# Optimization experiments

Hardware: AMD Instinct MI355X
Metric: run time of the kernel (lower is better)

Reference implementation:

```python
import jax, jax.numpy as jnp
import numpy as np

B, N, M, C = 2, 8192, 1024, 1152  # batch, dense points, centers, feature dim
K = 3                              # three_nn interpolation
EPS = 1e-8


def setup_inputs() -> dict:
    key = jax.random.key(0)
    k1, k2, k3 = jax.random.split(key, 3)
    xyz = jax.random.normal(k1, (B, N, 3), dtype=jnp.float32)      # query points
    center = jax.random.normal(k2, (B, M, 3), dtype=jnp.float32)   # center coords (already permuted to B,M,3)
    feats = jax.random.normal(k3, (B, C, M), dtype=jnp.float32)    # backbone features at centers
    return {"xyz": xyz, "center": center, "feats": feats}


def _interpolate(xyz, center, feats):
    # Squared pairwise distances [B, N, M] (PointNet++ three_nn uses squared dists).
    d2 = (jnp.sum(xyz * xyz, axis=-1, keepdims=True)
          + jnp.sum(center * center, axis=-1)[:, None, :]
          - 2.0 * jnp.einsum('bnd,bmd->bnm', xyz, center))
    neg_top, idx = jax.lax.top_k(-d2, K)          # 3 nearest centers per point
    dist = -neg_top                                # [B, N, K] squared distances
    recip = 1.0 / (dist + EPS)
    weight = recip / jnp.sum(recip, axis=-1, keepdims=True)  # [B, N, K]
    fm = jnp.transpose(feats, (0, 2, 1))           # [B, M, C]
    batch_idx = jnp.arange(B)[:, None, None]       # broadcast gather over batch
    gathered = fm[batch_idx, idx]                  # [B, N, K, C]
    out = jnp.einsum('bnkc,bnk->bcn', gathered, weight)  # [B, C, N]
    return out


def reference(xyz, center, feats):
    return _interpolate(xyz, center, feats)
```

## Files before the change

### kernel.cpp

```cpp
#include <hip/hip_runtime.h>
#include <cstdint>

#define B_ 2
#define N_ 8192
#define M_ 1024
#define C_ 1152
#define EPS_ 1e-8f
#define NT 32
#define CHUNK 128
#define NBN (N_ / NT)
#define NBC (C_ / CHUNK)
#define PTS 16
#define TRB ((M_ / 64) * (C_ / 64) * B_)

typedef float f32x4 __attribute__((ext_vector_type(4)));

__device__ __forceinline__ unsigned short f2bf(float f) {
    unsigned u = __float_as_uint(f);
    u += 0x7fffu + ((u >> 16) & 1u);
    return (unsigned short)(u >> 16);
}
__device__ __forceinline__ float bf2f(unsigned short h) {
    return __uint_as_float(((unsigned)h) << 16);
}

__device__ __forceinline__ void ins3lex(float d, int i,
        float& d0, int& i0, float& d1, int& i1, float& d2, int& i2) {
    bool b0 = (d < d0) || (d == d0 && i < i0);
    bool b1 = (d < d1) || (d == d1 && i < i1);
    bool b2 = (d < d2) || (d == d2 && i < i2);
    d2 = b1 ? d1 : (b2 ? d : d2);   i2 = b1 ? i1 : (b2 ? i : i2);
    d1 = b0 ? d0 : (b1 ? d : d1);   i1 = b0 ? i0 : (b1 ? i : i1);
    d0 = b0 ? d  : d0;              i0 = b0 ? i  : i0;
}

__global__ __launch_bounds__(256, 4) void k_front(const float* __restrict__ feats,
                                                  unsigned short* __restrict__ fm,
                                                  const float* __restrict__ xyz,
                                                  const float* __restrict__ center,
                                                  int* __restrict__ idx_ws,
                                                  float* __restrict__ w_ws) {
    __shared__ float4 sc[1040];
    int bid = blockIdx.x;
    int t   = threadIdx.x;

    if (bid < TRB) {
        float* tile = (float*)sc;
        int within = bid % ((M_ / 64) * (C_ / 64));
        int b  = bid / ((M_ / 64) * (C_ / 64));
        int mb = within & 15;
        int cb = within >> 4;
        int m0 = mb * 64;
        int c0 = cb * 64;
        int tx = t & 63;
        int ty = t >> 6;
        const float* src = feats + ((size_t)b * C_ + c0) * M_ + m0;
#pragma unroll
        for (int j = 0; j < 16; ++j) {
            int cl = ty + 4 * j;
            tile[cl * 65 + tx] = __builtin_nontemporal_load(&src[(size_t)cl * M_ + tx]);
        }
        __syncthreads();
        unsigned short* dst = fm + ((size_t)b * M_ + m0) * C_ + c0;
#pragma unroll
        for (int j = 0; j < 16; ++j) {
            int ml = ty + 4 * j;
            dst[(size_t)ml * C_ + tx] = f2bf(tile[tx * 65 + ml]);
        }
        return;
    }

    int flat = bid - TRB;
    int b    = flat >> 9;
    int n0   = (flat & 511) * PTS;
    for (int i = t; i < M_; i += 256) {
        float cx = center[((size_t)b * M_ + i) * 3 + 0];
        float cy = center[((size_t)b * M_ + i) * 3 + 1];
        float cz = center[((size_t)b * M_ + i) * 3 + 2];
        float cc = __fadd_rn(__fadd_rn(__fmul_rn(cx, cx), __fmul_rn(cy, cy)),
                             __fmul_rn(cz, cz));
        sc[i] = make_float4(cx, cy, cz, cc);
    }
    __syncthreads();

    int p = t >> 4;
    int c = t & 15;
    int n = n0 + p;
    float x = xyz[((size_t)b * N_ + n) * 3 + 0];
    float y = xyz[((size_t)b * N_ + n) * 3 + 1];
    float z = xyz[((size_t)b * N_ + n) * 3 + 2];
    float xx = __fadd_rn(__fadd_rn(__fmul_rn(x, x), __fmul_rn(y, y)),
                         __fmul_rn(z, z));

    float d0 = __builtin_inff(), d1 = __builtin_inff(), d2 = __builtin_inff();
    int   i0 = 0x7fffffff,  i1 = 0x7fffffff,  i2 = 0x7fffffff;
#pragma unroll
    for (int it = 0; it < 64; ++it) {
        float4 v = sc[c + it * 16];
        float dot = __fmaf_rn(z, v.z, __fmaf_rn(y, v.y, __fmul_rn(x, v.x)));
        float s0  = __fadd_rn(xx, v.w);
        float d   = __fmaf_rn(-2.0f, dot, s0);
        int   m   = c + it * 16;
        bool b0 = d < d0;
        bool b1 = d < d1;
        bool b2 = d < d2;
        float nd0 = fminf(d, d0);
        float nd1 = __builtin_amdgcn_fmed3f(d, d0, d1);
        float nd2 = __builtin_amdgcn_fmed3f(d, d1, d2);
        i2 = b1 ? i1 : (b2 ? m : i2);
        i1 = b0 ? i0 : (b1 ? m : i1);
        i0 = b0 ? m  : i0;
        d0 = nd0; d1 = nd1; d2 = nd2;
    }

#pragma unroll
    for (int off = 1; off <= 8; off <<= 1) {
        float e0 = __shfl_xor(d0, off); int j0 = __shfl_xor(i0, off);
        float e1 = __shfl_xor(d1, off); int j1 = __shfl_xor(i1, off);
        float e2 = __shfl_xor(d2, off); int j2 = __shfl_xor(i2, off);
        ins3lex(e0, j0, d0, i0, d1, i1, d2, i2);
        ins3lex(e1, j1, d0, i0, d1, i1, d2, i2);
        ins3lex(e2, j2, d0, i0, d1, i1, d2, i2);
    }
    if (c == 0) {
        float r0w = 1.0f / __fadd_rn(d0, EPS_);
        float r1w = 1.0f / __fadd_rn(d1, EPS_);
        float r2w = 1.0f / __fadd_rn(d2, EPS_);
        float s   = __fadd_rn(__fadd_rn(r0w, r1w), r2w);
        size_t base = ((size_t)b * N_ + n) * 3;
        idx_ws[base + 0] = i0; idx_ws[base + 1] = i1; idx_ws[base + 2] = i2;
        w_ws[base + 0] = r0w / s; w_ws[base + 1] = r1w / s; w_ws[base + 2] = r2w / s;
    }
}

__global__ __launch_bounds__(256) void k_interp(const unsigned short* __restrict__ fm,
                                                const int* __restrict__ idx_ws,
                                                const float* __restrict__ w_ws,
                                                float* __restrict__ out) {
    __shared__ float T[NT][CHUNK + 1];
    __shared__ int   sbase[NT][3];
    __shared__ float sw[NT][3];
    int flat = blockIdx.x;
    int slot = flat & 7;
    int b    = slot >> 2;
    int idx  = (flat >> 3) * 4 + (slot & 3);
    int n0   = (idx & (NBN - 1)) * NT;
    int c0   = (idx >> 8) * CHUNK;
    int t    = threadIdx.x;
    if (t < NT) {
        size_t ib = ((size_t)b * N_ + n0 + t) * 3;
#pragma unroll
        for (int k = 0; k < 3; ++k) {
            sbase[t][k] = (b * M_ + idx_ws[ib + k]) * C_;
            sw[t][k]    = w_ws[ib + k];
        }
    }
    __syncthreads();
    int wave = t >> 6;
    int lane = t & 63;
    int half = lane >> 5;
    int cl   = (lane & 31) * 4;
#pragma unroll
    for (int pp = 0; pp < 4; ++pp) {
        int p = pp * 8 + wave * 2 + half;
        float w0 = sw[p][0], w1 = sw[p][1], w2 = sw[p][2];
        const ushort4 a0 = *(const ushort4*)(fm + sbase[p][0] + c0 + cl);
        const ushort4 a1 = *(const ushort4*)(fm + sbase[p][1] + c0 + cl);
        const ushort4 a2 = *(const ushort4*)(fm + sbase[p][2] + c0 + cl);
        T[p][cl + 0] = __fmaf_rn(bf2f(a2.x), w2, __fmaf_rn(bf2f(a1.x), w1, __fmul_rn(bf2f(a0.x), w0)));
        T[p][cl + 1] = __fmaf_rn(bf2f(a2.y), w2, __fmaf_rn(bf2f(a1.y), w1, __fmul_rn(bf2f(a0.y), w0)));
        T[p][cl + 2] = __fmaf_rn(bf2f(a2.z), w2, __fmaf_rn(bf2f(a1.z), w1, __fmul_rn(bf2f(a0.z), w0)));
        T[p][cl + 3] = __fmaf_rn(bf2f(a2.w), w2, __fmaf_rn(bf2f(a1.w), w1, __fmul_rn(bf2f(a0.w), w0)));
    }
    __syncthreads();
    int p4  = (t & 7) * 4;
    int ccb = t >> 3;
#pragma unroll
    for (int r = 0; r < 4; ++r) {
        int cc = r * 32 + ccb;
        f32x4 v = { T[p4 + 0][cc], T[p4 + 1][cc], T[p4 + 2][cc], T[p4 + 3][cc] };
        __builtin_nontemporal_store(v,
            (f32x4*)&out[((size_t)b * C_ + c0 + cc) * N_ + n0 + p4]);
    }
}

extern "C" void kernel_launch(void* const* d_in, const int* in_sizes, int n_in,
                              void* d_out, int out_size, void* d_ws, size_t ws_size,
                              hipStream_t stream) {
    const float* xyz    = (const float*)d_in[0];
    const float* center = (const float*)d_in[1];
    const float* feats  = (const float*)d_in[2];
    float* out = (float*)d_out;

    char*           ws     = (char*)d_ws;
    unsigned short* fm     = (unsigned short*)ws;
    int*            idx_ws = (int*)(ws + (size_t)B_ * M_ * C_ * 2);
    float*          w_ws   = (float*)(ws + (size_t)B_ * M_ * C_ * 2 + (size_t)B_ * N_ * 3 * 4);

    k_front <<<TRB + (N_ / PTS) * B_, 256, 0, stream>>>(feats, fm, xyz, center, idx_ws, w_ws);
    k_interp<<<NBN * NBC * B_, 256, 0, stream>>>(fm, idx_ws, w_ws, out);
}
```

Baseline: 37.97 us.

## Split kNN center search across two blocks and merge candidates in interp

Each k_front kNN block now scans only half of the centers, so twice as many blocks run with half the shared-memory fill and loop length. Each writes its partial top-3 (distance and index) to a candidate buffer. k_interp merges the two candidate sets and computes the inverse-distance weights itself, which removes the separate idx/weight outputs. The kNN blocks now come before the transpose blocks in the grid, and the occupancy hint on launch bounds is dropped. The cost is extra candidate traffic and a merge that is repeated by every interp block reading the same points.

```diff
diff --git a/kernel.cpp b/kernel.cpp
--- a/kernel.cpp
+++ b/kernel.cpp
@@ -11,6 +11,9 @@
 #define NBN (N_ / NT)
 #define NBC (C_ / CHUNK)
 #define PTS 16
+#define NSL 2
+#define MSL (M_ / NSL)
+#define NNB ((N_ / PTS) * NSL * B_)
 #define TRB ((M_ / 64) * (C_ / 64) * B_)
 
 typedef float f32x4 __attribute__((ext_vector_type(4)));
@@ -34,20 +37,20 @@
     d0 = b0 ? d  : d0;              i0 = b0 ? i  : i0;
 }
 
-__global__ __launch_bounds__(256, 4) void k_front(const float* __restrict__ feats,
-                                                  unsigned short* __restrict__ fm,
-                                                  const float* __restrict__ xyz,
-                                                  const float* __restrict__ center,
-                                                  int* __restrict__ idx_ws,
-                                                  float* __restrict__ w_ws) {
-    __shared__ float4 sc[1040];
+__global__ __launch_bounds__(256) void k_front(const float* __restrict__ feats,
+                                               unsigned short* __restrict__ fm,
+                                               const float* __restrict__ xyz,
+                                               const float* __restrict__ center,
+                                               float* __restrict__ cand) {
+    __shared__ float4 shb[1040];
     int bid = blockIdx.x;
     int t   = threadIdx.x;
 
-    if (bid < TRB) {
-        float* tile = (float*)sc;
-        int within = bid % ((M_ / 64) * (C_ / 64));
-        int b  = bid / ((M_ / 64) * (C_ / 64));
+    if (bid >= NNB) {
+        float* tile = (float*)shb;
+        int tb = bid - NNB;
+        int within = tb % ((M_ / 64) * (C_ / 64));
+        int b  = tb / ((M_ / 64) * (C_ / 64));
         int mb = within & 15;
         int cb = within >> 4;
         int m0 = mb * 64;
@@ -70,16 +73,25 @@
         return;
     }
 
-    int flat = bid - TRB;
-    int b    = flat >> 9;
-    int n0   = (flat & 511) * PTS;
-    for (int i = t; i < M_; i += 256) {
-        float cx = center[((size_t)b * M_ + i) * 3 + 0];
-        float cy = center[((size_t)b * M_ + i) * 3 + 1];
-        float cz = center[((size_t)b * M_ + i) * 3 + 2];
-        float cc = __fadd_rn(__fadd_rn(__fmul_rn(cx, cx), __fmul_rn(cy, cy)),
-                             __fmul_rn(cz, cz));
-        sc[i] = make_float4(cx, cy, cz, cc);
+    float4* sc = shb;
+    int b      = bid >> 10;
+    int within = bid & 1023;
+    int pg     = within >> 1;
+    int s      = within & 1;
+    int n0     = pg * PTS;
+    int msl    = s * MSL;
+
+    {
+        int i0s = 2 * t;
+        const float* cp = center + ((size_t)b * M_ + msl + i0s) * 3;
+        float ax = cp[0], ay = cp[1], az = cp[2];
+        float bx = cp[3], by = cp[4], bz = cp[5];
+        float acc = __fadd_rn(__fadd_rn(__fmul_rn(ax, ax), __fmul_rn(ay, ay)),
+                              __fmul_rn(az, az));
+        float bcc = __fadd_rn(__fadd_rn(__fmul_rn(bx, bx), __fmul_rn(by, by)),
+                              __fmul_rn(bz, bz));
+        sc[i0s]     = make_float4(ax, ay, az, acc);
+        sc[i0s + 1] = make_float4(bx, by, bz, bcc);
     }
     __syncthreads();
 
@@ -94,13 +106,13 @@
 
     float d0 = __builtin_inff(), d1 = __builtin_inff(), d2 = __builtin_inff();
     int   i0 = 0x7fffffff,  i1 = 0x7fffffff,  i2 = 0x7fffffff;
-#pragma unroll
-    for (int it = 0; it < 64; ++it) {
+#pragma unroll 8
+    for (int it = 0; it < MSL / 16; ++it) {
         float4 v = sc[c + it * 16];
         float dot = __fmaf_rn(z, v.z, __fmaf_rn(y, v.y, __fmul_rn(x, v.x)));
         float s0  = __fadd_rn(xx, v.w);
         float d   = __fmaf_rn(-2.0f, dot, s0);
-        int   m   = c + it * 16;
+        int   m   = msl + c + it * 16;
         bool b0 = d < d0;
         bool b1 = d < d1;
         bool b2 = d < d2;
@@ -123,19 +135,15 @@
         ins3lex(e2, j2, d0, i0, d1, i1, d2, i2);
     }
     if (c == 0) {
-        float r0w = 1.0f / __fadd_rn(d0, EPS_);
-        float r1w = 1.0f / __fadd_rn(d1, EPS_);
-        float r2w = 1.0f / __fadd_rn(d2, EPS_);
-        float s   = __fadd_rn(__fadd_rn(r0w, r1w), r2w);
-        size_t base = ((size_t)b * N_ + n) * 3;
-        idx_ws[base + 0] = i0; idx_ws[base + 1] = i1; idx_ws[base + 2] = i2;
-        w_ws[base + 0] = r0w / s; w_ws[base + 1] = r1w / s; w_ws[base + 2] = r2w / s;
+        size_t base = (((size_t)b * N_ + n) * NSL + s) * 6;
+        cand[base + 0] = d0; ((int*)cand)[base + 1] = i0;
+        cand[base + 2] = d1; ((int*)cand)[base + 3] = i1;
+        cand[base + 4] = d2; ((int*)cand)[base + 5] = i2;
     }
 }
 
 __global__ __launch_bounds__(256) void k_interp(const unsigned short* __restrict__ fm,
-                                                const int* __restrict__ idx_ws,
-                                                const float* __restrict__ w_ws,
+                                                const float* __restrict__ cand,
                                                 float* __restrict__ out) {
     __shared__ float T[NT][CHUNK + 1];
     __shared__ int   sbase[NT][3];
@@ -148,12 +156,20 @@
     int c0   = (idx >> 8) * CHUNK;
     int t    = threadIdx.x;
     if (t < NT) {
-        size_t ib = ((size_t)b * N_ + n0 + t) * 3;
-#pragma unroll
-        for (int k = 0; k < 3; ++k) {
-            sbase[t][k] = (b * M_ + idx_ws[ib + k]) * C_;
-            sw[t][k]    = w_ws[ib + k];
-        }
+        size_t cb = ((size_t)b * N_ + n0 + t) * (NSL * 6);
+        float D0 = cand[cb + 0]; int I0 = ((const int*)cand)[cb + 1];
+        float D1 = cand[cb + 2]; int I1 = ((const int*)cand)[cb + 3];
+        float D2 = cand[cb + 4]; int I2 = ((const int*)cand)[cb + 5];
+        ins3lex(cand[cb + 6],  ((const int*)cand)[cb + 7],  D0, I0, D1, I1, D2, I2);
+        ins3lex(cand[cb + 8],  ((const int*)cand)[cb + 9],  D0, I0, D1, I1, D2, I2);
+        ins3lex(cand[cb + 10], ((const int*)cand)[cb + 11], D0, I0, D1, I1, D2, I2);
+        float r0 = 1.0f / __fadd_rn(D0, EPS_);
+        float r1 = 1.0f / __fadd_rn(D1, EPS_);
+        float r2 = 1.0f / __fadd_rn(D2, EPS_);
+        float s  = __fadd_rn(__fadd_rn(r0, r1), r2);
+        sbase[t][0] = (b * M_ + I0) * C_;  sw[t][0] = r0 / s;
+        sbase[t][1] = (b * M_ + I1) * C_;  sw[t][1] = r1 / s;
+        sbase[t][2] = (b * M_ + I2) * C_;  sw[t][2] = r2 / s;
     }
     __syncthreads();
     int wave = t >> 6;
@@ -192,11 +208,10 @@
     const float* feats  = (const float*)d_in[2];
     float* out = (float*)d_out;
 
-    char*           ws     = (char*)d_ws;
-    unsigned short* fm     = (unsigned short*)ws;
-    int*            idx_ws = (int*)(ws + (size_t)B_ * M_ * C_ * 2);
-    float*          w_ws   = (float*)(ws + (size_t)B_ * M_ * C_ * 2 + (size_t)B_ * N_ * 3 * 4);
-
-    k_front <<<TRB + (N_ / PTS) * B_, 256, 0, stream>>>(feats, fm, xyz, center, idx_ws, w_ws);
-    k_interp<<<NBN * NBC * B_, 256, 0, stream>>>(fm, idx_ws, w_ws, out);
-}
+    char*           ws   = (char*)d_ws;
+    unsigned short* fm   = (unsigned short*)ws;
+    float*          cand = (float*)(ws + (size_t)B_ * M_ * C_ * 2);
+
+    k_front <<<NNB + TRB, 256, 0, stream>>>(feats, fm, xyz, center, cand);
+    k_interp<<<NBN * NBC * B_, 256, 0, stream>>>(fm, cand, out);
+}
```

Result: faster. 36.01 us (median of 2 runs) (-5.2%).
